# Kernel optimization log

Measured on AMD Instinct MI355X. Metric: run time of the kernel, lower is better.

The kernel has to match this reference:

```python
import jax, jax.numpy as jnp
import numpy as np

B, N, D = 2, 2048, 1024
H = 16
HD = D // H  # 64
N_CTX = 256


def setup_inputs() -> dict:
    key = jax.random.key(0)
    ks = jax.random.split(key, 10)
    x = jax.random.normal(ks[0], (B, N, D), dtype=jnp.float32)
    ctx_ppr = jax.random.uniform(ks[1], (N_CTX,), dtype=jnp.float32, minval=1e-4, maxval=1.0)
    ctx_trust = jax.random.uniform(ks[2], (N_CTX,), dtype=jnp.float32)
    attn_mask = jax.random.randint(ks[3], (N, N), 0, 2).astype(jnp.bool_)
    # parameters (nn.Linear convention: y = x @ W.T + b)
    s_in = 1.0 / np.sqrt(D)
    W_in = jax.random.uniform(ks[4], (3 * D, D), dtype=jnp.float32, minval=-s_in, maxval=s_in)
    b_in = jax.random.uniform(ks[5], (3 * D,), dtype=jnp.float32, minval=-s_in, maxval=s_in)
    W_out = jax.random.uniform(ks[6], (D, D), dtype=jnp.float32, minval=-s_in, maxval=s_in)
    b_out = jax.random.uniform(ks[7], (D,), dtype=jnp.float32, minval=-s_in, maxval=s_in)
    log_ppr_alpha = jnp.ones((1,), jnp.float32) * 0.1
    trust_scale = jnp.ones((1,), jnp.float32) * 0.1
    return {"x": x, "ctx_ppr": ctx_ppr, "ctx_trust": ctx_trust, "n_ctx": N_CTX,
            "attn_mask": attn_mask, "W_in": W_in, "b_in": b_in,
            "W_out": W_out, "b_out": b_out,
            "log_ppr_alpha": log_ppr_alpha, "trust_scale": trust_scale}


def reference(x, ctx_ppr, ctx_trust, n_ctx, attn_mask, W_in, b_in, W_out, b_out,
              log_ppr_alpha, trust_scale):
    Bx, Nx, Dx = x.shape
    scale = HD ** -0.5
    qkv = x @ W_in.T + b_in  # [B,N,3D]
    q, k, v = jnp.split(qkv, 3, axis=-1)
    q = q.reshape(Bx, Nx, H, HD).transpose(0, 2, 1, 3)  # [B,H,N,d]
    k = k.reshape(Bx, Nx, H, HD).transpose(0, 2, 1, 3)
    v = v.reshape(Bx, Nx, H, HD).transpose(0, 2, 1, 3)
    if n_ctx > 0:
        gate = jax.nn.sigmoid(trust_scale[0] * ctx_trust)  # [n_ctx]
        gate_full = jnp.concatenate([gate, jnp.ones(Nx - n_ctx, x.dtype)])
        v = v * gate_full[None, None, :, None]
    logits = jnp.einsum('bhqd,bhkd->bhqk', q, k) * scale
    if n_ctx > 0:
        bias = log_ppr_alpha[0] * jnp.log(jnp.clip(ctx_ppr, 1e-8, None))
        col_bias = jnp.concatenate([bias, jnp.zeros(Nx - n_ctx, x.dtype)])
        logits = logits + col_bias[None, None, None, :]
    logits = jnp.where(attn_mask[None, None, :, :], -jnp.inf, logits)
    weights = jax.nn.softmax(logits, axis=-1)
    out = jnp.einsum('bhqk,bhkd->bhqd', weights, v)
    out = out.transpose(0, 2, 1, 3).reshape(Bx, Nx, Dx)
    return out @ W_out.T + b_out
```

## Files before the change

kernel.cpp:

```cpp
#include <hip/hip_runtime.h>
#include <hip/hip_bf16.h>
#include <hip/hip_fp16.h>
#include <math.h>

#define B_   2
#define N_   2048
#define D_   1024
#define H_   16
#define TD_  3072
#define LOG2E 1.44269504088896340736f
#define SCALE_Q (0.125f * LOG2E)

typedef short  bf16x8 __attribute__((ext_vector_type(8)));
typedef _Float16 f16x8 __attribute__((ext_vector_type(8)));
typedef float  f32x4  __attribute__((ext_vector_type(4)));
typedef float  f32x16 __attribute__((ext_vector_type(16)));

#define MFMA16(a, b, c)   __builtin_amdgcn_mfma_f32_16x16x32_bf16(a, b, c, 0, 0, 0)
#define MFMA32B(a, b, c)  __builtin_amdgcn_mfma_f32_32x32x16_bf16(a, b, c, 0, 0, 0)
#define MFMA32H(a, b, c)  __builtin_amdgcn_mfma_f32_32x32x16_f16(a, b, c, 0, 0, 0)

__device__ __forceinline__ ushort f2bf(float f) {
    union { float f; unsigned u; } v; v.f = f;
    unsigned r = (v.u + 0x7fffu + ((v.u >> 16) & 1u)) >> 16;
    return (ushort)r;
}
__device__ __forceinline__ unsigned pkrtz(float a, float b) {
    typedef __fp16 h2 __attribute__((ext_vector_type(2)));
    union { h2 h; unsigned u; } c;
    c.h = __builtin_amdgcn_cvt_pkrtz(a, b);
    return c.u;
}
__device__ __forceinline__ void async16(const void* g, void* l) {
    __builtin_amdgcn_global_load_lds(
        (const __attribute__((address_space(1))) unsigned*)g,
        (__attribute__((address_space(3))) unsigned*)l, 16, 0, 0);
}

__global__ __launch_bounds__(256) void preprocess(
    const float* __restrict__ x, const float* __restrict__ W_in,
    const float* __restrict__ W_out, const float* __restrict__ ctx_ppr,
    const float* __restrict__ log_alpha, const int* __restrict__ n_ctx_p,
    const int* __restrict__ mask,
    ushort* __restrict__ xb, ushort* __restrict__ wib, ushort* __restrict__ wob,
    float* __restrict__ biasrow, unsigned* __restrict__ maskbits)
{
    const int J0 = 1048576, J1 = 786432, J2 = 262144, JM = 131072, JB = 2048;
    int t = blockIdx.x * 256 + threadIdx.x;
    if (t < J0 + J1 + J2) {
        const float* src; ushort* dst; int i = t;
        if (i < J0)           { src = x;      dst = xb;  }
        else if (i < J0 + J1) { i -= J0;      src = W_in;  dst = wib; }
        else                  { i -= J0 + J1; src = W_out; dst = wob; }
        float4 v = ((const float4*)src)[i];
        ushort4 o;
        o.x = f2bf(v.x); o.y = f2bf(v.y); o.z = f2bf(v.z); o.w = f2bf(v.w);
        ((ushort4*)dst)[i] = o;
    } else if (t < J0 + J1 + J2 + JM) {
        int i = t - (J0 + J1 + J2);
        const int4* m = (const int4*)(mask + (size_t)i * 32);
        unsigned bits = 0u;
        #pragma unroll
        for (int j = 0; j < 8; ++j) {
            int4 w = m[j];
            bits |= (w.x != 0 ? 1u : 0u) << (j * 4 + 0);
            bits |= (w.y != 0 ? 1u : 0u) << (j * 4 + 1);
            bits |= (w.z != 0 ? 1u : 0u) << (j * 4 + 2);
            bits |= (w.w != 0 ? 1u : 0u) << (j * 4 + 3);
        }
        maskbits[i] = bits;
    } else if (t < J0 + J1 + J2 + JM + JB) {
        int k = t - (J0 + J1 + J2 + JM);
        int nc = n_ctx_p[0];
        float bv = -4.f;
        if (k < nc) bv = log_alpha[0] * __log2f(fmaxf(ctx_ppr[k], 1e-8f)) - 4.f;
        biasrow[k] = bv;
    }
}

template<int BCOL, int MODE>
__global__ __launch_bounds__(256) void gemm_bt(
    const ushort* __restrict__ A, const ushort* __restrict__ Bw,
    const float* __restrict__ bias, float* __restrict__ Cf,
    ushort* __restrict__ Ch, int Ncol, int K,
    const float* __restrict__ ctx_trust, const float* __restrict__ trust_scale,
    const int* __restrict__ n_ctx_p)
{
    constexpr int NT = BCOL / 32;
    __shared__ ushort tA[128 * 32];
    __shared__ ushort tB[BCOL * 32];
    const int tid = threadIdx.x;
    const int lane = tid & 63, wv = tid >> 6;
    const int ln = lane & 15, kg = lane >> 4;
    const int rh = wv >> 1, ch = wv & 1;
    const int row0 = blockIdx.y * 128, col0 = blockIdx.x * BCOL;

    int offA[4], offB[NT];
    #pragma unroll
    for (int i = 0; i < 4; ++i) {
        int ra = rh * 64 + i * 16 + ln;
        offA[i] = ra * 32 + ((kg ^ ((ra >> 1) & 3)) << 3);
    }
    #pragma unroll
    for (int i = 0; i < NT; ++i) {
        int rb = ch * (BCOL / 2) + i * 16 + ln;
        offB[i] = rb * 32 + ((kg ^ ((rb >> 1) & 3)) << 3);
    }
    f32x4 acc[4][NT];
    #pragma unroll
    for (int i = 0; i < 4; ++i)
        #pragma unroll
        for (int j = 0; j < NT; ++j) acc[i][j] = (f32x4){0.f, 0.f, 0.f, 0.f};

    for (int kt = 0; kt < K; kt += 32) {
        __syncthreads();
        #pragma unroll
        for (int r2 = 0; r2 < 2; ++r2) {
            int g = r2 * 256 + tid;
            int row = g >> 2;
            int srck = ((g & 3) ^ ((row >> 1) & 3)) << 3;
            async16(A + (size_t)(row0 + row) * K + kt + srck, &tA[g * 8]);
        }
        #pragma unroll
        for (int r2 = 0; r2 < BCOL / 64; ++r2) {
            int g = r2 * 256 + tid;
            int row = g >> 2;
            int srck = ((g & 3) ^ ((row >> 1) & 3)) << 3;
            async16(Bw + (size_t)(col0 + row) * K + kt + srck, &tB[g * 8]);
        }
        __syncthreads();
        bf16x8 af[4], bfr[NT];
        #pragma unroll
        for (int i = 0; i < 4; ++i)  af[i]  = *(const bf16x8*)&tA[offA[i]];
        #pragma unroll
        for (int i = 0; i < NT; ++i) bfr[i] = *(const bf16x8*)&tB[offB[i]];
        #pragma unroll
        for (int mt = 0; mt < 4; ++mt)
            #pragma unroll
            for (int nt = 0; nt < NT; ++nt)
                acc[mt][nt] = MFMA16(af[mt], bfr[nt], acc[mt][nt]);
    }

    const int nctx = n_ctx_p ? n_ctx_p[0] : 0;
    const float ts = trust_scale ? trust_scale[0] : 0.f;
    #pragma unroll
    for (int nt = 0; nt < NT; ++nt) {
        int col = col0 + ch * (BCOL / 2) + nt * 16 + ln;
        float cbv = (MODE != 2) ? bias[col] : 0.f;
        float gmul = 1.f;
        if (MODE == 2) {
            int tok = col & (N_ - 1);
            if (tok < nctx)
                gmul = 1.f / (1.f + __expf(-ts * ctx_trust[tok]));
        }
        #pragma unroll
        for (int mt = 0; mt < 4; ++mt) {
            int rbase = row0 + rh * 64 + mt * 16 + kg * 4;
            f32x4 a = acc[mt][nt];
            if (MODE == 0) {
                #pragma unroll
                for (int reg = 0; reg < 4; ++reg)
                    Cf[(size_t)(rbase + reg) * Ncol + col] = a[reg] + cbv;
            } else if (MODE == 1) {
                const float qs = (col < D_) ? SCALE_Q : 1.f;
                #pragma unroll
                for (int reg = 0; reg < 4; ++reg)
                    Ch[(size_t)(rbase + reg) * Ncol + col] = f2bf((a[reg] + cbv) * qs);
            } else {
                f32x4 bv4 = *(const f32x4*)&bias[rbase];
                #pragma unroll
                for (int reg = 0; reg < 4; ++reg) {
                    float v = (a[reg] + bv4[reg]) * gmul;
                    _Float16 hv = (_Float16)v;
                    union { _Float16 h; ushort u; } cv; cv.h = hv;
                    Ch[((size_t)((col >> 11) * 1024 + rbase + reg)) * 2048 + (col & (N_ - 1))] = cv.u;
                }
            }
        }
    }
}

__global__ __launch_bounds__(512, 4) void attn(
    const ushort* __restrict__ qkb,
    const _Float16* __restrict__ vT,
    const unsigned* __restrict__ maskbits,
    const float* __restrict__ biasrow,
    float* __restrict__ pO,
    float* __restrict__ pl)
{
    __shared__ ushort   Kt[2][64 * 64];
    __shared__ _Float16 Vt[2][64 * 64];
    const int tid = threadIdx.x;
    const int lane = tid & 63, wv = tid >> 6;
    const int q31 = lane & 31, hi = lane >> 5;
    const int bh = blockIdx.x;
    const int b = bh >> 4, h = bh & 15;
    const int z = blockIdx.z;
    const int k0z = z * 512;
    const int q = blockIdx.y * 256 + wv * 32 + q31;

    bf16x8 qf[4];
    {
        const ushort* qrow = qkb + (size_t)(b * N_ + q) * 2048 + h * 64;
        #pragma unroll
        for (int ks = 0; ks < 4; ++ks)
            qf[ks] = *(const bf16x8*)(qrow + ks * 16 + hi * 8);
    }
    const size_t kgbase = (size_t)(b * N_) * 2048 + 1024 + h * 64;
    const _Float16* vbase = vT + (size_t)(b * 1024 + h * 64) * 2048;

    f32x16 O[2];
    O[0] = (f32x16)(0.f); O[1] = (f32x16)(0.f);
    float lrun = 0.f;

    {
        int g = tid; int row = g >> 3;
        int sg = (g & 7) ^ ((row ^ (row >> 3)) & 7);
        async16(qkb + kgbase + (size_t)(k0z + row) * 2048 + sg * 8, &Kt[0][g * 8]);
        async16(vbase + (size_t)row * 2048 + k0z + sg * 8, &Vt[0][g * 8]);
    }

    int fsw[2];
    #pragma unroll
    for (int t = 0; t < 2; ++t) {
        int row = t * 32 + q31;
        fsw[t] = (row ^ (row >> 3)) & 7;
    }

    for (int ci = 0; ci < 8; ++ci) {
        const int c0 = ci * 64;
        __syncthreads();
        if (ci < 7) {
            const int c1 = c0 + 64, nb = (ci + 1) & 1;
            int g = tid; int row = g >> 3;
            int sg = (g & 7) ^ ((row ^ (row >> 3)) & 7);
            async16(qkb + kgbase + (size_t)(k0z + c1 + row) * 2048 + sg * 8, &Kt[nb][g * 8]);
            async16(vbase + (size_t)row * 2048 + k0z + c1 + sg * 8, &Vt[nb][g * 8]);
        }
        const ushort*   KT = Kt[ci & 1];
        const _Float16* VT = Vt[ci & 1];

        uint2 mw = *(const uint2*)&maskbits[(size_t)q * 64 + z * 16 + ci * 2];
        unsigned msh[2] = { mw.x >> (hi * 4), mw.y >> (hi * 4) };
        f32x4 bb[2][4];
        #pragma unroll
        for (int t = 0; t < 2; ++t)
            #pragma unroll
            for (int g = 0; g < 4; ++g)
                bb[t][g] = *(const f32x4*)&biasrow[k0z + c0 + t * 32 + g * 8 + hi * 4];

        f32x16 S[2];
        S[0] = (f32x16)(0.f); S[1] = (f32x16)(0.f);
        #pragma unroll
        for (int t = 0; t < 2; ++t) {
            const int rbase = (t * 32 + q31) * 64;
            #pragma unroll
            for (int ks = 0; ks < 4; ++ks) {
                bf16x8 kf = *(const bf16x8*)&KT[rbase + (((ks * 2 + hi) ^ fsw[t]) << 3)];
                S[t] = MFMA32B(kf, qf[ks], S[t]);
            }
        }

        unsigned pk[2][8];
        __half2 hs0 = __float2half2_rn(0.f), hs1 = __float2half2_rn(0.f);
        #pragma unroll
        for (int t = 0; t < 2; ++t) {
            float p[16];
            #pragma unroll
            for (int g = 0; g < 4; ++g)
                #pragma unroll
                for (int r = 0; r < 4; ++r) {
                    const int reg = g * 4 + r;
                    const int br = r + 8 * g;
                    float s = S[t][reg] + bb[t][g][r];
                    s = ((msh[t] >> br) & 1u) ? -1e30f : s;
                    p[reg] = __builtin_exp2f(s);
                }
            #pragma unroll
            for (int i = 0; i < 8; ++i) {
                pk[t][i] = pkrtz(p[2 * i], p[2 * i + 1]);
                union { unsigned u; __half2 h; } c; c.u = pk[t][i];
                if (i & 1) hs1 = __hadd2(hs1, c.h); else hs0 = __hadd2(hs0, c.h);
            }
        }
        {
            __half2 hs = __hadd2(hs0, hs1);
            lrun += __low2float(hs) + __high2float(hs);
        }

        #pragma unroll
        for (int ks = 0; ks < 4; ++ks) {
            const int t = ks >> 1, lo4 = (ks & 1) * 4;
            unsigned u0 = pk[t][lo4 + 0], u1 = pk[t][lo4 + 1];
            unsigned u2 = pk[t][lo4 + 2], u3 = pk[t][lo4 + 3];
            unsigned own0 = hi ? u2 : u0, own1 = hi ? u3 : u1;
            unsigned snd0 = hi ? u0 : u2, snd1 = hi ? u1 : u3;
            unsigned rv0 = (unsigned)__shfl_xor((int)snd0, 32);
            unsigned rv1 = (unsigned)__shfl_xor((int)snd1, 32);
            union { f16x8 v; unsigned u[4]; } frag;
            frag.u[0] = hi ? rv0 : own0;
            frag.u[1] = hi ? rv1 : own1;
            frag.u[2] = hi ? own0 : rv0;
            frag.u[3] = hi ? own1 : rv1;
            #pragma unroll
            for (int t2 = 0; t2 < 2; ++t2) {
                const int vb = (t2 * 32 + q31) * 64;
                union { f16x8 v; int4 i; } vf;
                vf.i = *(const int4*)&VT[vb + (((ks * 2 + hi) ^ fsw[t2]) << 3)];
                O[t2] = MFMA32H(vf.v, frag.v, O[t2]);
            }
        }
    }

    float* obase = pO + (((size_t)(z * 32 + bh) * 2048) + q) * 64;
    #pragma unroll
    for (int t = 0; t < 2; ++t)
        #pragma unroll
        for (int g = 0; g < 4; ++g) {
            f32x4 o4 = { O[t][g * 4 + 0], O[t][g * 4 + 1], O[t][g * 4 + 2], O[t][g * 4 + 3] };
            *(f32x4*)(obase + t * 32 + g * 8 + hi * 4) = o4;
        }
    float l = lrun + __shfl_xor(lrun, 32);
    if (hi == 0)
        pl[(size_t)(z * 32 + bh) * 2048 + q] = l;
}

__global__ __launch_bounds__(256) void combine(
    const float* __restrict__ pO, const float* __restrict__ pl,
    ushort* __restrict__ attb)
{
    const size_t ZSTR = (size_t)32 * 2048 * 64;
    int i = blockIdx.x * 256 + threadIdx.x;
    int bhq = i >> 4, d4 = (i & 15) << 2;
    const float* o0 = pO + (size_t)bhq * 64 + d4;
    float l = pl[bhq] + pl[bhq + 65536] + pl[bhq + 131072] + pl[bhq + 196608];
    float inv = 1.f / l;
    f32x4 a0 = *(const f32x4*)o0;
    f32x4 a1 = *(const f32x4*)(o0 + ZSTR);
    f32x4 a2 = *(const f32x4*)(o0 + 2 * ZSTR);
    f32x4 a3 = *(const f32x4*)(o0 + 3 * ZSTR);
    ushort4 o;
    #pragma unroll
    for (int r = 0; r < 4; ++r)
        ((ushort*)&o)[r] = f2bf(((a0[r] + a1[r]) + (a2[r] + a3[r])) * inv);
    int bh = bhq >> 11, q = bhq & 2047;
    *(ushort4*)&attb[((size_t)((bh >> 4) * 2048 + q)) * 1024 + (bh & 15) * 64 + d4] = o;
}

extern "C" void kernel_launch(void* const* d_in, const int* in_sizes, int n_in,
                              void* d_out, int out_size, void* d_ws, size_t ws_size,
                              hipStream_t stream)
{
    const float* x         = (const float*)d_in[0];
    const float* ctx_ppr   = (const float*)d_in[1];
    const float* ctx_trust = (const float*)d_in[2];
    const int*   n_ctx_p   = (const int*)d_in[3];
    const int*   attn_mask = (const int*)d_in[4];
    const float* W_in      = (const float*)d_in[5];
    const float* b_in      = (const float*)d_in[6];
    const float* W_out     = (const float*)d_in[7];
    const float* b_out     = (const float*)d_in[8];
    const float* log_alpha = (const float*)d_in[9];
    const float* trust_sc  = (const float*)d_in[10];
    float* out = (float*)d_out;

    char* ws = (char*)d_ws;
    float*     pO     = (float*)ws;
    ushort*    xb     = (ushort*)ws;
    ushort*    wib    = (ushort*)(ws + (size_t)4096 * 1024 * 2);
    ws += (size_t)4 * 32 * 2048 * 64 * 4;
    float*     pl     = (float*)ws;     ws += (size_t)4 * 32 * 2048 * 4;
    ushort*    qkb    = (ushort*)ws;    ws += (size_t)4096 * 2048 * 2;
    _Float16*  vT     = (_Float16*)ws;  ws += (size_t)2048 * 2048 * 2;
    ushort*    attbuf = (ushort*)ws;    ws += (size_t)4096 * 1024 * 2;
    ushort*    wob    = (ushort*)ws;    ws += (size_t)1024 * 1024 * 2;
    unsigned*  maskbits = (unsigned*)ws; ws += (size_t)2048 * 64 * 4;
    float*     biasrow  = (float*)ws;    ws += 2048 * 4;

    hipLaunchKernelGGL(preprocess, dim3(8712), dim3(256), 0, stream,
                       x, W_in, W_out, ctx_ppr, log_alpha, n_ctx_p, attn_mask,
                       xb, wib, wob, biasrow, maskbits);

    hipLaunchKernelGGL((gemm_bt<128, 1>), dim3(16, 32), dim3(256), 0, stream,
                       xb, wib, b_in, (float*)nullptr, qkb, 2048, 1024,
                       (const float*)nullptr, (const float*)nullptr, (const int*)nullptr);

    hipLaunchKernelGGL((gemm_bt<64, 2>), dim3(64, 8), dim3(256), 0, stream,
                       wib + (size_t)2048 * 1024, xb, b_in + 2 * D_, (float*)nullptr,
                       (ushort*)vT, 4096, 1024, ctx_trust, trust_sc, n_ctx_p);

    hipLaunchKernelGGL(attn, dim3(32, 8, 4), dim3(512), 0, stream,
                       qkb, vT, maskbits, biasrow, pO, pl);

    hipLaunchKernelGGL(combine, dim3(4096), dim3(256), 0, stream,
                       pO, pl, attbuf);

    hipLaunchKernelGGL((gemm_bt<64, 0>), dim3(16, 32), dim3(256), 0, stream,
                       attbuf, wob, b_out, out, (ushort*)nullptr, 1024, 1024,
                       (const float*)nullptr, (const float*)nullptr, (const int*)nullptr);
}
```

Measured before the change: 277.8 us.

## Halve attention key splits, skip bias outside context, use shuffle-free f16 PV MFMA

Key-dimension splits in the attention kernel drop from four to two, so each block loops over 16 key chunks. This halves the partial-output traffic and the work in the combine kernel. Bias loads and adds now run only for chunks that overlap the context prefix. The PV product switches from cross-lane shuffles with the 32x32x16 f16 MFMA to the 32x32x8 f16 MFMA fed directly from each lane's packed probabilities, and the row sum is accumulated in fp32 instead of fp16. The -4 exponent offset is removed from the bias. Fewer blocks reduces parallelism and may raise the risk of fp16 overflow in the probabilities.

```diff
diff --git a/kernel.cpp b/kernel.cpp
--- a/kernel.cpp
+++ b/kernel.cpp
@@ -13,12 +13,14 @@
 
 typedef short  bf16x8 __attribute__((ext_vector_type(8)));
 typedef _Float16 f16x8 __attribute__((ext_vector_type(8)));
+typedef _Float16 f16x4 __attribute__((ext_vector_type(4)));
+typedef float  f32x2  __attribute__((ext_vector_type(2)));
 typedef float  f32x4  __attribute__((ext_vector_type(4)));
 typedef float  f32x16 __attribute__((ext_vector_type(16)));
 
 #define MFMA16(a, b, c)   __builtin_amdgcn_mfma_f32_16x16x32_bf16(a, b, c, 0, 0, 0)
 #define MFMA32B(a, b, c)  __builtin_amdgcn_mfma_f32_32x32x16_bf16(a, b, c, 0, 0, 0)
-#define MFMA32H(a, b, c)  __builtin_amdgcn_mfma_f32_32x32x16_f16(a, b, c, 0, 0, 0)
+#define MFMA328(a, b, c)  __builtin_amdgcn_mfma_f32_32x32x8f16(a, b, c, 0, 0, 0)
 
 __device__ __forceinline__ ushort f2bf(float f) {
     union { float f; unsigned u; } v; v.f = f;
@@ -72,8 +74,8 @@
     } else if (t < J0 + J1 + J2 + JM + JB) {
         int k = t - (J0 + J1 + J2 + JM);
         int nc = n_ctx_p[0];
-        float bv = -4.f;
-        if (k < nc) bv = log_alpha[0] * __log2f(fmaxf(ctx_ppr[k], 1e-8f)) - 4.f;
+        float bv = 0.f;
+        if (k < nc) bv = log_alpha[0] * __log2f(fmaxf(ctx_ppr[k], 1e-8f));
         biasrow[k] = bv;
     }
 }
@@ -185,6 +187,7 @@
     const _Float16* __restrict__ vT,
     const unsigned* __restrict__ maskbits,
     const float* __restrict__ biasrow,
+    const int* __restrict__ n_ctx_p,
     float* __restrict__ pO,
     float* __restrict__ pl)
 {
@@ -196,8 +199,9 @@
     const int bh = blockIdx.x;
     const int b = bh >> 4, h = bh & 15;
     const int z = blockIdx.z;
-    const int k0z = z * 512;
+    const int k0z = z * 1024;
     const int q = blockIdx.y * 256 + wv * 32 + q31;
+    const int nctx = n_ctx_p[0];
 
     bf16x8 qf[4];
     {
@@ -227,10 +231,10 @@
         fsw[t] = (row ^ (row >> 3)) & 7;
     }
 
-    for (int ci = 0; ci < 8; ++ci) {
+    for (int ci = 0; ci < 16; ++ci) {
         const int c0 = ci * 64;
         __syncthreads();
-        if (ci < 7) {
+        if (ci < 15) {
             const int c1 = c0 + 64, nb = (ci + 1) & 1;
             int g = tid; int row = g >> 3;
             int sg = (g & 7) ^ ((row ^ (row >> 3)) & 7);
@@ -240,14 +244,9 @@
         const ushort*   KT = Kt[ci & 1];
         const _Float16* VT = Vt[ci & 1];
 
-        uint2 mw = *(const uint2*)&maskbits[(size_t)q * 64 + z * 16 + ci * 2];
+        uint2 mw = *(const uint2*)&maskbits[(size_t)q * 64 + z * 32 + ci * 2];
         unsigned msh[2] = { mw.x >> (hi * 4), mw.y >> (hi * 4) };
-        f32x4 bb[2][4];
-        #pragma unroll
-        for (int t = 0; t < 2; ++t)
-            #pragma unroll
-            for (int g = 0; g < 4; ++g)
-                bb[t][g] = *(const f32x4*)&biasrow[k0z + c0 + t * 32 + g * 8 + hi * 4];
+        const bool has_bias = (k0z + c0) < nctx;
 
         f32x16 S[2];
         S[0] = (f32x16)(0.f); S[1] = (f32x16)(0.f);
@@ -262,54 +261,58 @@
         }
 
         unsigned pk[2][8];
-        __half2 hs0 = __float2half2_rn(0.f), hs1 = __float2half2_rn(0.f);
+        f32x2 ls = (f32x2){0.f, 0.f};
         #pragma unroll
         for (int t = 0; t < 2; ++t) {
             float p[16];
-            #pragma unroll
-            for (int g = 0; g < 4; ++g)
-                #pragma unroll
-                for (int r = 0; r < 4; ++r) {
-                    const int reg = g * 4 + r;
-                    const int br = r + 8 * g;
-                    float s = S[t][reg] + bb[t][g][r];
-                    s = ((msh[t] >> br) & 1u) ? -1e30f : s;
-                    p[reg] = __builtin_exp2f(s);
+            if (has_bias) {
+                #pragma unroll
+                for (int g = 0; g < 4; ++g) {
+                    f32x4 bb = *(const f32x4*)&biasrow[k0z + c0 + t * 32 + g * 8 + hi * 4];
+                    #pragma unroll
+                    for (int r = 0; r < 4; ++r) {
+                        const int reg = g * 4 + r;
+                        const int br = r + 8 * g;
+                        float s = S[t][reg] + bb[r];
+                        s = ((msh[t] >> br) & 1u) ? -1e30f : s;
+                        p[reg] = __builtin_exp2f(s);
+                    }
                 }
+            } else {
+                #pragma unroll
+                for (int g = 0; g < 4; ++g)
+                    #pragma unroll
+                    for (int r = 0; r < 4; ++r) {
+                        const int reg = g * 4 + r;
+                        const int br = r + 8 * g;
+                        float s = S[t][reg];
+                        s = ((msh[t] >> br) & 1u) ? -1e30f : s;
+                        p[reg] = __builtin_exp2f(s);
+                    }
+            }
             #pragma unroll
             for (int i = 0; i < 8; ++i) {
                 pk[t][i] = pkrtz(p[2 * i], p[2 * i + 1]);
-                union { unsigned u; __half2 h; } c; c.u = pk[t][i];
-                if (i & 1) hs1 = __hadd2(hs1, c.h); else hs0 = __hadd2(hs0, c.h);
+                ls += (f32x2){p[2 * i], p[2 * i + 1]};
             }
         }
-        {
-            __half2 hs = __hadd2(hs0, hs1);
-            lrun += __low2float(hs) + __high2float(hs);
-        }
-
-        #pragma unroll
-        for (int ks = 0; ks < 4; ++ks) {
-            const int t = ks >> 1, lo4 = (ks & 1) * 4;
-            unsigned u0 = pk[t][lo4 + 0], u1 = pk[t][lo4 + 1];
-            unsigned u2 = pk[t][lo4 + 2], u3 = pk[t][lo4 + 3];
-            unsigned own0 = hi ? u2 : u0, own1 = hi ? u3 : u1;
-            unsigned snd0 = hi ? u0 : u2, snd1 = hi ? u1 : u3;
-            unsigned rv0 = (unsigned)__shfl_xor((int)snd0, 32);
-            unsigned rv1 = (unsigned)__shfl_xor((int)snd1, 32);
-            union { f16x8 v; unsigned u[4]; } frag;
-            frag.u[0] = hi ? rv0 : own0;
-            frag.u[1] = hi ? rv1 : own1;
-            frag.u[2] = hi ? own0 : rv0;
-            frag.u[3] = hi ? own1 : rv1;
+        lrun += ls[0] + ls[1];
+
+        #pragma unroll
+        for (int t = 0; t < 2; ++t)
             #pragma unroll
-            for (int t2 = 0; t2 < 2; ++t2) {
-                const int vb = (t2 * 32 + q31) * 64;
-                union { f16x8 v; int4 i; } vf;
-                vf.i = *(const int4*)&VT[vb + (((ks * 2 + hi) ^ fsw[t2]) << 3)];
-                O[t2] = MFMA32H(vf.v, frag.v, O[t2]);
+            for (int s = 0; s < 4; ++s) {
+                union { f16x4 v; unsigned u[2]; } pf;
+                pf.u[0] = pk[t][2 * s];
+                pf.u[1] = pk[t][2 * s + 1];
+                #pragma unroll
+                for (int t2 = 0; t2 < 2; ++t2) {
+                    union { f16x4 v; uint2 i; } vf;
+                    vf.i = *(const uint2*)&VT[(t2 * 32 + q31) * 64 +
+                                              ((((t << 2) + s) ^ fsw[t2]) << 3) + (hi << 2)];
+                    O[t2] = MFMA328(vf.v, pf.v, O[t2]);
+                }
             }
-        }
     }
 
     float* obase = pO + (((size_t)(z * 32 + bh) * 2048) + q) * 64;
@@ -333,16 +336,14 @@
     int i = blockIdx.x * 256 + threadIdx.x;
     int bhq = i >> 4, d4 = (i & 15) << 2;
     const float* o0 = pO + (size_t)bhq * 64 + d4;
-    float l = pl[bhq] + pl[bhq + 65536] + pl[bhq + 131072] + pl[bhq + 196608];
+    float l = pl[bhq] + pl[bhq + 65536];
     float inv = 1.f / l;
     f32x4 a0 = *(const f32x4*)o0;
     f32x4 a1 = *(const f32x4*)(o0 + ZSTR);
-    f32x4 a2 = *(const f32x4*)(o0 + 2 * ZSTR);
-    f32x4 a3 = *(const f32x4*)(o0 + 3 * ZSTR);
     ushort4 o;
     #pragma unroll
     for (int r = 0; r < 4; ++r)
-        ((ushort*)&o)[r] = f2bf(((a0[r] + a1[r]) + (a2[r] + a3[r])) * inv);
+        ((ushort*)&o)[r] = f2bf((a0[r] + a1[r]) * inv);
     int bh = bhq >> 11, q = bhq & 2047;
     *(ushort4*)&attb[((size_t)((bh >> 4) * 2048 + q)) * 1024 + (bh & 15) * 64 + d4] = o;
 }
@@ -368,8 +369,8 @@
     float*     pO     = (float*)ws;
     ushort*    xb     = (ushort*)ws;
     ushort*    wib    = (ushort*)(ws + (size_t)4096 * 1024 * 2);
-    ws += (size_t)4 * 32 * 2048 * 64 * 4;
-    float*     pl     = (float*)ws;     ws += (size_t)4 * 32 * 2048 * 4;
+    ws += (size_t)2 * 32 * 2048 * 64 * 4;
+    float*     pl     = (float*)ws;     ws += (size_t)2 * 32 * 2048 * 4;
     ushort*    qkb    = (ushort*)ws;    ws += (size_t)4096 * 2048 * 2;
     _Float16*  vT     = (_Float16*)ws;  ws += (size_t)2048 * 2048 * 2;
     ushort*    attbuf = (ushort*)ws;    ws += (size_t)4096 * 1024 * 2;
@@ -389,8 +390,8 @@
                        wib + (size_t)2048 * 1024, xb, b_in + 2 * D_, (float*)nullptr,
                        (ushort*)vT, 4096, 1024, ctx_trust, trust_sc, n_ctx_p);
 
-    hipLaunchKernelGGL(attn, dim3(32, 8, 4), dim3(512), 0, stream,
-                       qkb, vT, maskbits, biasrow, pO, pl);
+    hipLaunchKernelGGL(attn, dim3(32, 8, 2), dim3(512), 0, stream,
+                       qkb, vT, maskbits, biasrow, n_ctx_p, pO, pl);
 
     hipLaunchKernelGGL(combine, dim3(4096), dim3(256), 0, stream,
                        pO, pl, attbuf);
```

Result: slower. 302.0 us (+8.7%).
